# Kernel optimization log

Measured on AMD Instinct MI355X. Metric: run time of the kernel, lower is better.

The kernel has to match this reference:

```python
import jax, jax.numpy as jnp
import numpy as np

DIM = 768
MID = 256
HEADS = 12
P_SCALE = 0.8
SCALE = (DIM // HEADS) ** -0.5


def setup_inputs() -> dict:
    key = jax.random.key(0)
    ks = jax.random.split(key, 9)
    B, N, C = 64, 197, DIM
    s = 0.02
    return {
        "x": jax.random.normal(ks[0], (B, N, C), jnp.float32),
        "qkv_w": jax.random.normal(ks[1], (3 * C, C), jnp.float32) * s,
        "qkv_b": jax.random.normal(ks[2], (3 * C,), jnp.float32) * s,
        "proj_w": jax.random.normal(ks[3], (C, C), jnp.float32) * s,
        "proj_b": jax.random.normal(ks[4], (C,), jnp.float32) * s,
        "down_w": jax.random.normal(ks[5], (MID, C), jnp.float32) * s,
        "down_b": jax.random.normal(ks[6], (MID,), jnp.float32) * s,
        "up_w": jax.random.normal(ks[7], (2 * C, MID), jnp.float32) * s,
        "up_b": jax.random.normal(ks[8], (2 * C,), jnp.float32) * s,
    }


def reference(x, qkv_w, qkv_b, proj_w, proj_b, down_w, down_b, up_w, up_b):
    B, N, C = x.shape
    H, D = HEADS, C // HEADS
    # Adapter: down -> tanh -> up gives kv prefix; q prefix is zeros
    kv_prefix = jnp.tanh(x @ down_w.T + down_b) @ up_w.T + up_b  # [B,N,2C]
    prefix = jnp.concatenate([jnp.zeros((B, N, C), x.dtype), kv_prefix], -1)
    qkv = (x @ qkv_w.T + qkv_b) + P_SCALE * prefix  # [B,N,3C]
    qkv = qkv.reshape(B, N, 3, H, D).transpose(2, 0, 3, 1, 4)  # [3,B,H,N,D]
    q, k, v = qkv[0], qkv[1], qkv[2]
    attn = jax.nn.softmax(jnp.einsum("bhnd,bhmd->bhnm", q, k) * SCALE, axis=-1)
    out = jnp.einsum("bhnm,bhmd->bhnd", attn, v)  # [B,H,N,D]
    out = out.transpose(0, 2, 1, 3).reshape(B, N, C)
    return out @ proj_w.T + proj_b
```

## Files before the change

### kernel.cpp

```cpp
#include <hip/hip_runtime.h>
#include <hip/hip_bf16.h>
#include <stdint.h>

#define DIM   768
#define MID   256
#define HEADS 12
#define NB    64
#define NN    197
#define NT    (NB*NN)
#define QKVC  2304
#define NCOMB 2560

typedef __attribute__((ext_vector_type(4))) float f32x4;
typedef __attribute__((ext_vector_type(8))) short s8v;

__device__ __forceinline__ unsigned short f2b(float f) {
    union { float f; unsigned int u; } x; x.f = f;
    unsigned int u = x.u;
    unsigned int r = (u + 0x7FFFu + ((u >> 16) & 1u)) >> 16;
    return (unsigned short)r;
}
__device__ __forceinline__ float b2f(unsigned short s) {
    union { unsigned int u; float f; } x; x.u = ((unsigned int)s) << 16;
    return x.f;
}

__device__ __forceinline__ void gld_lds16(const void* g, void* l) {
    __builtin_amdgcn_global_load_lds(
        (const __attribute__((address_space(1))) unsigned int*)g,
        (__attribute__((address_space(3))) unsigned int*)l, 16, 0, 0);
}

__global__ void cast_f32_bf16(const float* __restrict__ in,
                              unsigned short* __restrict__ out, int n4) {
    int i = blockIdx.x * blockDim.x + threadIdx.x;
    int stride = gridDim.x * blockDim.x;
    for (; i < n4; i += stride) {
        float4 v = ((const float4*)in)[i];
        ushort4 o;
        o.x = f2b(v.x); o.y = f2b(v.y); o.z = f2b(v.z); o.w = f2b(v.w);
        ((ushort4*)out)[i] = o;
    }
}

__global__ void cast_weights(const float* __restrict__ qkv_w,
                             const float* __restrict__ down_w,
                             const float* __restrict__ up_w,
                             const float* __restrict__ proj_w,
                             unsigned short* __restrict__ o_comb,
                             unsigned short* __restrict__ o_up,
                             unsigned short* __restrict__ o_proj) {
    int blk = blockIdx.x;
    const float* in; unsigned short* out; int base;
    if (blk < 1728)      { in = qkv_w;  out = o_comb;                  base = blk; }
    else if (blk < 1920) { in = down_w; out = o_comb + QKVC * DIM;     base = blk - 1728; }
    else if (blk < 2304) { in = up_w;   out = o_up;                    base = blk - 1920; }
    else                 { in = proj_w; out = o_proj;                  base = blk - 2304; }
    int i = base * 256 + threadIdx.x;
    float4 v = ((const float4*)in)[i];
    ushort4 o;
    o.x = f2b(v.x); o.y = f2b(v.y); o.z = f2b(v.z); o.w = f2b(v.w);
    ((ushort4*)out)[i] = o;
}

__global__ __launch_bounds__(512) void gemm256k64(
    const unsigned short* __restrict__ A,
    const unsigned short* __restrict__ W,
    const float* __restrict__ bias0,
    const float* __restrict__ bias1,
    int M, int K, int GN,
    unsigned short* __restrict__ qkvbuf,
    unsigned short* __restrict__ hbuf)
{
    __shared__ __align__(16) unsigned short As[2][256][64];
    __shared__ __align__(16) unsigned short Bs[2][256][64];
    const int tid = threadIdx.x;
    const int l = tid & 63;
    const int w = tid >> 6;
    const int wr = w >> 2, wc = w & 3;

    const int nwg = gridDim.x;
    const int orig = blockIdx.x;
    const int q8 = nwg >> 3, r8 = nwg & 7;
    const int xcd = orig & 7, slice = orig >> 3;
    const int wgid = (xcd < r8 ? xcd * (q8 + 1)
                               : r8 * (q8 + 1) + (xcd - r8) * q8) + slice;
    const int bm = wgid / GN;
    const int bn = wgid - bm * GN;

    f32x4 acc[8][4];
#pragma unroll
    for (int m = 0; m < 8; ++m)
#pragma unroll
        for (int n = 0; n < 4; ++n)
            acc[m][n] = (f32x4){0.f, 0.f, 0.f, 0.f};

    const int KT = K >> 6;
    const int sc = (((tid & 7) ^ ((tid >> 3) & 7)) << 3);
    const int dc = ((tid & 7) << 3);
    const int rr = tid >> 3;

    auto stage = [&](int buf, int kt) {
        const int k0 = kt << 6;
#pragma unroll
        for (int p = 0; p < 4; ++p) {
            int r = p * 64 + rr;
            int ra = bm * 256 + r; if (ra > M - 1) ra = M - 1;
            gld_lds16(A + (size_t)ra * K + k0 + sc, &As[buf][r][dc]);
            int rb = bn * 256 + r;
            gld_lds16(W + (size_t)rb * K + k0 + sc, &Bs[buf][r][dc]);
        }
    };

    stage(0, 0);

    const int ar  = l & 15;
    const int ch0 = (((l >> 4)    ) ^ (l & 7)) << 3;
    const int ch1 = (((l >> 4) + 4) ^ (l & 7)) << 3;

    for (int t = 0; t < KT; ++t) {
        const int cur = t & 1;
        if (t + 1 < KT) {
            stage(cur ^ 1, t + 1);
            asm volatile("s_waitcnt vmcnt(8)" ::: "memory");
        } else {
            asm volatile("s_waitcnt vmcnt(0)" ::: "memory");
        }
        __builtin_amdgcn_s_barrier();
#pragma unroll
        for (int kk = 0; kk < 2; ++kk) {
            const int ch = kk ? ch1 : ch0;
            s8v a[8], b[4];
#pragma unroll
            for (int m = 0; m < 8; ++m)
                a[m] = *(const s8v*)&As[cur][wr * 128 + m * 16 + ar][ch];
#pragma unroll
            for (int n = 0; n < 4; ++n)
                b[n] = *(const s8v*)&Bs[cur][wc * 64 + n * 16 + ar][ch];
            __builtin_amdgcn_s_setprio(1);
#pragma unroll
            for (int m = 0; m < 8; ++m)
#pragma unroll
                for (int n = 0; n < 4; ++n)
                    acc[m][n] = __builtin_amdgcn_mfma_f32_16x16x32_bf16(a[m], b[n], acc[m][n], 0, 0, 0);
            __builtin_amdgcn_s_setprio(0);
        }
        __builtin_amdgcn_s_barrier();
    }
    asm volatile("s_waitcnt vmcnt(0)" ::: "memory");
    __builtin_amdgcn_s_barrier();

    unsigned short* stg = ((unsigned short*)&As[0][0][0]) + w * (16 * 68);
    const int cbase = bn * 256 + wc * 64;
    const bool ish = (cbase >= QKVC);
#pragma unroll
    for (int mq = 0; mq < 8; ++mq) {
#pragma unroll
        for (int n = 0; n < 4; ++n) {
            int c = cbase + n * 16 + (l & 15);
            float bi = ish ? bias1[c - QKVC] : bias0[c];
            float sc2 = (c < DIM) ? 0.125f : 1.0f;
#pragma unroll
            for (int j = 0; j < 4; ++j) {
                float v = acc[mq][n][j] + bi;
                v = ish ? tanhf(v) : v * sc2;
                stg[((l >> 4) * 4 + j) * 68 + n * 16 + (l & 15)] = f2b(v);
            }
        }
#pragma unroll
        for (int p = 0; p < 2; ++p) {
            int rr2 = p * 8 + (l >> 3);
            int r = bm * 256 + wr * 128 + mq * 16 + rr2;
            s8v v = *(const s8v*)&stg[rr2 * 68 + (l & 7) * 8];
            if (r < M) {
                if (!ish) *(s8v*)&qkvbuf[(size_t)r * QKVC + cbase + (l & 7) * 8] = v;
                else      *(s8v*)&hbuf[(size_t)r * MID + (cbase - QKVC) + (l & 7) * 8] = v;
            }
        }
    }
}

template<int EPI>
__global__ __launch_bounds__(256) void gemm_bt(
    const unsigned short* __restrict__ A,
    const unsigned short* __restrict__ W,
    const float* __restrict__ bias,
    int M, int K, int GN,
    unsigned short* __restrict__ qkvbuf,
    float* __restrict__ outf)
{
    __shared__ __align__(16) unsigned short lds[2][2][128 * 32];
    const int tid = threadIdx.x;
    const int l = tid & 63;
    const int w = tid >> 6;
    const int wr = w >> 1, wc = w & 1;

    const int nwg = gridDim.x;
    const int orig = blockIdx.x;
    const int q8 = nwg >> 3, r8 = nwg & 7;
    const int xcd = orig & 7, slice = orig >> 3;
    const int wgid = (xcd < r8 ? xcd * (q8 + 1)
                               : r8 * (q8 + 1) + (xcd - r8) * q8) + slice;
    const int bm = wgid / GN;
    const int bn = wgid - bm * GN;

    f32x4 acc[4][4];
#pragma unroll
    for (int m = 0; m < 4; ++m)
#pragma unroll
        for (int n = 0; n < 4; ++n)
            acc[m][n] = (f32x4){0.f, 0.f, 0.f, 0.f};

    const int KT = K >> 5;

    auto stage = [&](int buf, int kt) {
        const int k0 = kt * 32;
        const int src = (((tid & 3) ^ ((tid >> 3) & 3)) << 3);
        const int dst = ((tid & 3) << 3);
#pragma unroll
        for (int p = 0; p < 2; ++p) {
            int r = p * 64 + (tid >> 2);
            int ra = bm * 128 + r; if (ra > M - 1) ra = M - 1;
            gld_lds16(A + (size_t)ra * K + k0 + src, &lds[buf][0][r * 32 + dst]);
            int rb = bn * 128 + r;
            gld_lds16(W + (size_t)rb * K + k0 + src, &lds[buf][1][r * 32 + dst]);
        }
    };

    stage(0, 0);
    __syncthreads();
    int buf = 0;
    const int rsl = (((l >> 4) ^ ((l >> 1) & 3)) << 3);
    for (int kt = 0; kt < KT; ++kt) {
        if (kt + 1 < KT) stage(buf ^ 1, kt + 1);
        const unsigned short* la = lds[buf][0];
        const unsigned short* lb = lds[buf][1];
        s8v a[4], b[4];
#pragma unroll
        for (int m = 0; m < 4; ++m)
            a[m] = *(const s8v*)&la[(wr * 64 + m * 16 + (l & 15)) * 32 + rsl];
#pragma unroll
        for (int n = 0; n < 4; ++n)
            b[n] = *(const s8v*)&lb[(wc * 64 + n * 16 + (l & 15)) * 32 + rsl];
#pragma unroll
        for (int m = 0; m < 4; ++m)
#pragma unroll
            for (int n = 0; n < 4; ++n)
                acc[m][n] = __builtin_amdgcn_mfma_f32_16x16x32_bf16(a[m], b[n], acc[m][n], 0, 0, 0);
        __syncthreads();
        buf ^= 1;
    }

    if (EPI == 1) {
        unsigned short* stg = ((unsigned short*)lds) + w * (16 * 68);
        const int C0 = bn * 128 + wc * 64;
#pragma unroll
        for (int mq = 0; mq < 4; ++mq) {
#pragma unroll
            for (int n = 0; n < 4; ++n) {
                int c = C0 + n * 16 + (l & 15);
                float bi = bias[c];
#pragma unroll
                for (int j = 0; j < 4; ++j)
                    stg[((l >> 4) * 4 + j) * 68 + n * 16 + (l & 15)] =
                        f2b(0.8f * (acc[mq][n][j] + bi));
            }
#pragma unroll
            for (int p = 0; p < 2; ++p) {
                int rr2 = p * 8 + (l >> 3);
                int r = bm * 128 + wr * 64 + mq * 16 + rr2;
                if (r < M) {
                    size_t base = (size_t)r * QKVC + DIM + C0 + (l & 7) * 8;
                    s8v add = *(const s8v*)&stg[rr2 * 68 + (l & 7) * 8];
                    s8v old = *(const s8v*)&qkvbuf[base];
                    s8v res;
#pragma unroll
                    for (int i = 0; i < 8; ++i)
                        res[i] = (short)f2b(b2f((unsigned short)old[i]) +
                                            b2f((unsigned short)add[i]));
                    *(s8v*)&qkvbuf[base] = res;
                }
            }
        }
    } else {
#pragma unroll
        for (int n = 0; n < 4; ++n) {
            int c = bn * 128 + wc * 64 + n * 16 + (l & 15);
            float bi = bias[c];
#pragma unroll
            for (int m = 0; m < 4; ++m) {
#pragma unroll
                for (int j = 0; j < 4; ++j) {
                    int r = bm * 128 + wr * 64 + m * 16 + (l >> 4) * 4 + j;
                    if (r >= M) continue;
                    outf[(size_t)r * DIM + c] = acc[m][n][j] + bi;
                }
            }
        }
    }
}

#define NKV  224
#define VPAD 232

__global__ __launch_bounds__(256) void attn_kernel(
    const unsigned short* __restrict__ qkv,
    unsigned short* __restrict__ ob)
{
    __shared__ __align__(16) unsigned short Ks[NKV * 64];
    __shared__ __align__(16) unsigned short Vt[64 * VPAD];
    __shared__ __align__(16) unsigned short Ps[64 * VPAD];

    const int tid = threadIdx.x;
    const int l = tid & 63;
    const int w = tid >> 6;
    const int bh = blockIdx.x;
    const int b = bh / HEADS, h = bh - b * HEADS;
    const unsigned short* qp = qkv + (size_t)(b * NN) * QKVC + h * 64;
    const unsigned short* kp = qp + DIM;
    const unsigned short* vp = qp + 2 * DIM;

    const s8v zer = (s8v){0, 0, 0, 0, 0, 0, 0, 0};

    for (int e = tid; e < NKV * 8; e += 256) {
        int r = e >> 3, ch = e & 7;
        int idx = (r * 64 + ch * 8) ^ ((r & 7) << 3);
        s8v val = (r < NN) ? *(const s8v*)&kp[(size_t)r * QKVC + ch * 8] : zer;
        *(s8v*)&Ks[idx] = val;
    }
    for (int e = tid; e < NKV * 8; e += 256) {
        int r = e >> 3, ch = e & 7;
        s8v val = (r < NN) ? *(const s8v*)&vp[(size_t)r * QKVC + ch * 8] : zer;
#pragma unroll
        for (int i = 0; i < 8; ++i)
            Vt[(ch * 8 + i) * VPAD + r] = (unsigned short)val[i];
    }
    __syncthreads();

    for (int qc = 0; qc < 4; ++qc) {
        const int rbase = qc * 64 + w * 16;
        s8v aq[2];
#pragma unroll
        for (int kc = 0; kc < 2; ++kc) {
            int r = rbase + (l & 15); if (r > NN - 1) r = NN - 1;
            aq[kc] = *(const s8v*)&qp[(size_t)r * QKVC + kc * 32 + (l >> 4) * 8];
        }
        f32x4 sacc[14];
#pragma unroll
        for (int t = 0; t < 14; ++t) sacc[t] = (f32x4){0.f, 0.f, 0.f, 0.f};
#pragma unroll
        for (int t = 0; t < 14; ++t) {
            int col = t * 16 + (l & 15);
#pragma unroll
            for (int kc = 0; kc < 2; ++kc) {
                int idx = (col * 64 + kc * 32 + (l >> 4) * 8) ^ ((col & 7) << 3);
                s8v bk = *(const s8v*)&Ks[idx];
                sacc[t] = __builtin_amdgcn_mfma_f32_16x16x32_bf16(aq[kc], bk, sacc[t], 0, 0, 0);
            }
        }
        float mx[4] = {-1e30f, -1e30f, -1e30f, -1e30f};
#pragma unroll
        for (int t = 0; t < 14; ++t) {
            int col = t * 16 + (l & 15);
            if (col < NN) {
#pragma unroll
                for (int j = 0; j < 4; ++j) mx[j] = fmaxf(mx[j], sacc[t][j]);
            }
        }
#pragma unroll
        for (int j = 0; j < 4; ++j)
#pragma unroll
            for (int off = 1; off < 16; off <<= 1)
                mx[j] = fmaxf(mx[j], __shfl_xor(mx[j], off, 64));

        float sm[4] = {0.f, 0.f, 0.f, 0.f};
#pragma unroll
        for (int t = 0; t < 14; ++t) {
            int col = t * 16 + (l & 15);
#pragma unroll
            for (int j = 0; j < 4; ++j) {
                float p = (col < NN) ? __expf(sacc[t][j] - mx[j]) : 0.f;
                sm[j] += p;
                Ps[(w * 16 + (l >> 4) * 4 + j) * VPAD + col] = f2b(p);
            }
        }
#pragma unroll
        for (int j = 0; j < 4; ++j)
#pragma unroll
            for (int off = 1; off < 16; off <<= 1)
                sm[j] += __shfl_xor(sm[j], off, 64);

        f32x4 oacc[4];
#pragma unroll
        for (int n = 0; n < 4; ++n) oacc[n] = (f32x4){0.f, 0.f, 0.f, 0.f};
#pragma unroll
        for (int kc = 0; kc < 7; ++kc) {
            s8v ap = *(const s8v*)&Ps[(w * 16 + (l & 15)) * VPAD + kc * 32 + (l >> 4) * 8];
#pragma unroll
            for (int n = 0; n < 4; ++n) {
                s8v bv = *(const s8v*)&Vt[(n * 16 + (l & 15)) * VPAD + kc * 32 + (l >> 4) * 8];
                oacc[n] = __builtin_amdgcn_mfma_f32_16x16x32_bf16(ap, bv, oacc[n], 0, 0, 0);
            }
        }
#pragma unroll
        for (int n = 0; n < 4; ++n) {
#pragma unroll
            for (int j = 0; j < 4; ++j) {
                int r = rbase + (l >> 4) * 4 + j;
                if (r < NN) {
                    float val = oacc[n][j] / sm[j];
                    ob[((size_t)(b * NN + r)) * DIM + h * 64 + n * 16 + (l & 15)] = f2b(val);
                }
            }
        }
    }
}

extern "C" void kernel_launch(void* const* d_in, const int* in_sizes, int n_in,
                              void* d_out, int out_size, void* d_ws, size_t ws_size,
                              hipStream_t stream) {
    const float* x      = (const float*)d_in[0];
    const float* qkv_w  = (const float*)d_in[1];
    const float* qkv_b  = (const float*)d_in[2];
    const float* proj_w = (const float*)d_in[3];
    const float* proj_b = (const float*)d_in[4];
    const float* down_w = (const float*)d_in[5];
    const float* down_b = (const float*)d_in[6];
    const float* up_w   = (const float*)d_in[7];
    const float* up_b   = (const float*)d_in[8];
    float* out = (float*)d_out;

    char* ws = (char*)d_ws;
    size_t off = 0;
    unsigned short* xb      = (unsigned short*)(ws + off); off += (size_t)NT * DIM * 2;
    unsigned short* wcomb   = (unsigned short*)(ws + off); off += (size_t)NCOMB * DIM * 2;
    unsigned short* up_wb   = (unsigned short*)(ws + off); off += (size_t)2 * DIM * MID * 2;
    unsigned short* proj_wb = (unsigned short*)(ws + off); off += (size_t)DIM * DIM * 2;
    unsigned short* hbuf    = (unsigned short*)(ws + off); off += (size_t)NT * MID * 2;
    unsigned short* qkvbuf  = (unsigned short*)(ws + off); off += (size_t)NT * QKVC * 2;
    unsigned short* obuf    = xb;

    cast_f32_bf16<<<2048, 256, 0, stream>>>(x, xb, NT * DIM / 4);
    cast_weights<<<2880, 256, 0, stream>>>(qkv_w, down_w, up_w, proj_w,
                                           wcomb, up_wb, proj_wb);

    const int GM1 = (NT + 127) / 128;
    const int GM2 = (NT + 255) / 256;
    gemm256k64<<<GM2 * (NCOMB / 256), 512, 0, stream>>>(xb, wcomb, qkv_b, down_b,
                                                        NT, DIM, NCOMB / 256, qkvbuf, hbuf);
    gemm_bt<1><<<GM1 * (2 * DIM / 128), 256, 0, stream>>>(hbuf, up_wb, up_b, NT, MID, 2 * DIM / 128,
                                                          qkvbuf, nullptr);
    attn_kernel<<<NB * HEADS, 256, 0, stream>>>(qkvbuf, obuf);
    gemm_bt<2><<<GM1 * (DIM / 128), 256, 0, stream>>>(obuf, proj_wb, proj_b, NT, DIM, DIM / 128,
                                                      nullptr, out);
}
```

Baseline: 230.9 us.

## Replace 256x256 QKV/down GEMM with generic 128x128 gemm_bt kernel

Removes the dedicated 512-thread 256x256-tile GEMM for the fused qkv+down projection and instead runs it through the templated 128x128 gemm_bt kernel with a new epilogue (bias, scale, tanh, split outputs). Smaller tiles give about four times as many workgroups, which improves load balance, but reduce operand reuse per byte loaded. The biases are now passed as two pointers throughout.

```diff
diff --git a/kernel.cpp b/kernel.cpp
--- a/kernel.cpp
+++ b/kernel.cpp
@@ -63,130 +63,15 @@
     ((ushort4*)out)[i] = o;
 }
 
-__global__ __launch_bounds__(512) void gemm256k64(
+template<int EPI>
+__global__ __launch_bounds__(256) void gemm_bt(
     const unsigned short* __restrict__ A,
     const unsigned short* __restrict__ W,
     const float* __restrict__ bias0,
     const float* __restrict__ bias1,
     int M, int K, int GN,
-    unsigned short* __restrict__ qkvbuf,
-    unsigned short* __restrict__ hbuf)
-{
-    __shared__ __align__(16) unsigned short As[2][256][64];
-    __shared__ __align__(16) unsigned short Bs[2][256][64];
-    const int tid = threadIdx.x;
-    const int l = tid & 63;
-    const int w = tid >> 6;
-    const int wr = w >> 2, wc = w & 3;
-
-    const int nwg = gridDim.x;
-    const int orig = blockIdx.x;
-    const int q8 = nwg >> 3, r8 = nwg & 7;
-    const int xcd = orig & 7, slice = orig >> 3;
-    const int wgid = (xcd < r8 ? xcd * (q8 + 1)
-                               : r8 * (q8 + 1) + (xcd - r8) * q8) + slice;
-    const int bm = wgid / GN;
-    const int bn = wgid - bm * GN;
-
-    f32x4 acc[8][4];
-#pragma unroll
-    for (int m = 0; m < 8; ++m)
-#pragma unroll
-        for (int n = 0; n < 4; ++n)
-            acc[m][n] = (f32x4){0.f, 0.f, 0.f, 0.f};
-
-    const int KT = K >> 6;
-    const int sc = (((tid & 7) ^ ((tid >> 3) & 7)) << 3);
-    const int dc = ((tid & 7) << 3);
-    const int rr = tid >> 3;
-
-    auto stage = [&](int buf, int kt) {
-        const int k0 = kt << 6;
-#pragma unroll
-        for (int p = 0; p < 4; ++p) {
-            int r = p * 64 + rr;
-            int ra = bm * 256 + r; if (ra > M - 1) ra = M - 1;
-            gld_lds16(A + (size_t)ra * K + k0 + sc, &As[buf][r][dc]);
-            int rb = bn * 256 + r;
-            gld_lds16(W + (size_t)rb * K + k0 + sc, &Bs[buf][r][dc]);
-        }
-    };
-
-    stage(0, 0);
-
-    const int ar  = l & 15;
-    const int ch0 = (((l >> 4)    ) ^ (l & 7)) << 3;
-    const int ch1 = (((l >> 4) + 4) ^ (l & 7)) << 3;
-
-    for (int t = 0; t < KT; ++t) {
-        const int cur = t & 1;
-        if (t + 1 < KT) {
-            stage(cur ^ 1, t + 1);
-            asm volatile("s_waitcnt vmcnt(8)" ::: "memory");
-        } else {
-            asm volatile("s_waitcnt vmcnt(0)" ::: "memory");
-        }
-        __builtin_amdgcn_s_barrier();
-#pragma unroll
-        for (int kk = 0; kk < 2; ++kk) {
-            const int ch = kk ? ch1 : ch0;
-            s8v a[8], b[4];
-#pragma unroll
-            for (int m = 0; m < 8; ++m)
-                a[m] = *(const s8v*)&As[cur][wr * 128 + m * 16 + ar][ch];
-#pragma unroll
-            for (int n = 0; n < 4; ++n)
-                b[n] = *(const s8v*)&Bs[cur][wc * 64 + n * 16 + ar][ch];
-            __builtin_amdgcn_s_setprio(1);
-#pragma unroll
-            for (int m = 0; m < 8; ++m)
-#pragma unroll
-                for (int n = 0; n < 4; ++n)
-                    acc[m][n] = __builtin_amdgcn_mfma_f32_16x16x32_bf16(a[m], b[n], acc[m][n], 0, 0, 0);
-            __builtin_amdgcn_s_setprio(0);
-        }
-        __builtin_amdgcn_s_barrier();
-    }
-    asm volatile("s_waitcnt vmcnt(0)" ::: "memory");
-    __builtin_amdgcn_s_barrier();
-
-    unsigned short* stg = ((unsigned short*)&As[0][0][0]) + w * (16 * 68);
-    const int cbase = bn * 256 + wc * 64;
-    const bool ish = (cbase >= QKVC);
-#pragma unroll
-    for (int mq = 0; mq < 8; ++mq) {
-#pragma unroll
-        for (int n = 0; n < 4; ++n) {
-            int c = cbase + n * 16 + (l & 15);
-            float bi = ish ? bias1[c - QKVC] : bias0[c];
-            float sc2 = (c < DIM) ? 0.125f : 1.0f;
-#pragma unroll
-            for (int j = 0; j < 4; ++j) {
-                float v = acc[mq][n][j] + bi;
-                v = ish ? tanhf(v) : v * sc2;
-                stg[((l >> 4) * 4 + j) * 68 + n * 16 + (l & 15)] = f2b(v);
-            }
-        }
-#pragma unroll
-        for (int p = 0; p < 2; ++p) {
-            int rr2 = p * 8 + (l >> 3);
-            int r = bm * 256 + wr * 128 + mq * 16 + rr2;
-            s8v v = *(const s8v*)&stg[rr2 * 68 + (l & 7) * 8];
-            if (r < M) {
-                if (!ish) *(s8v*)&qkvbuf[(size_t)r * QKVC + cbase + (l & 7) * 8] = v;
-                else      *(s8v*)&hbuf[(size_t)r * MID + (cbase - QKVC) + (l & 7) * 8] = v;
-            }
-        }
-    }
-}
-
-template<int EPI>
-__global__ __launch_bounds__(256) void gemm_bt(
-    const unsigned short* __restrict__ A,
-    const unsigned short* __restrict__ W,
-    const float* __restrict__ bias,
-    int M, int K, int GN,
-    unsigned short* __restrict__ qkvbuf,
+    unsigned short* __restrict__ ob0,
+    unsigned short* __restrict__ ob1,
     float* __restrict__ outf)
 {
     __shared__ __align__(16) unsigned short lds[2][2][128 * 32];
@@ -251,15 +136,44 @@
         buf ^= 1;
     }
 
-    if (EPI == 1) {
+    if (EPI == 0) {
         unsigned short* stg = ((unsigned short*)lds) + w * (16 * 68);
         const int C0 = bn * 128 + wc * 64;
+        const bool ish = (C0 >= QKVC);
 #pragma unroll
         for (int mq = 0; mq < 4; ++mq) {
 #pragma unroll
             for (int n = 0; n < 4; ++n) {
                 int c = C0 + n * 16 + (l & 15);
-                float bi = bias[c];
+                float bi = ish ? bias1[c - QKVC] : bias0[c];
+                float sc2 = (c < DIM) ? 0.125f : 1.0f;
+#pragma unroll
+                for (int j = 0; j < 4; ++j) {
+                    float v = acc[mq][n][j] + bi;
+                    v = ish ? tanhf(v) : v * sc2;
+                    stg[((l >> 4) * 4 + j) * 68 + n * 16 + (l & 15)] = f2b(v);
+                }
+            }
+#pragma unroll
+            for (int p = 0; p < 2; ++p) {
+                int rr2 = p * 8 + (l >> 3);
+                int r = bm * 128 + wr * 64 + mq * 16 + rr2;
+                s8v v = *(const s8v*)&stg[rr2 * 68 + (l & 7) * 8];
+                if (r < M) {
+                    if (!ish) *(s8v*)&ob0[(size_t)r * QKVC + C0 + (l & 7) * 8] = v;
+                    else      *(s8v*)&ob1[(size_t)r * MID + (C0 - QKVC) + (l & 7) * 8] = v;
+                }
+            }
+        }
+    } else if (EPI == 1) {
+        unsigned short* stg = ((unsigned short*)lds) + w * (16 * 68);
+        const int C0 = bn * 128 + wc * 64;
+#pragma unroll
+        for (int mq = 0; mq < 4; ++mq) {
+#pragma unroll
+            for (int n = 0; n < 4; ++n) {
+                int c = C0 + n * 16 + (l & 15);
+                float bi = bias0[c];
 #pragma unroll
                 for (int j = 0; j < 4; ++j)
                     stg[((l >> 4) * 4 + j) * 68 + n * 16 + (l & 15)] =
@@ -272,13 +186,13 @@
                 if (r < M) {
                     size_t base = (size_t)r * QKVC + DIM + C0 + (l & 7) * 8;
                     s8v add = *(const s8v*)&stg[rr2 * 68 + (l & 7) * 8];
-                    s8v old = *(const s8v*)&qkvbuf[base];
+                    s8v old = *(const s8v*)&ob0[base];
                     s8v res;
 #pragma unroll
                     for (int i = 0; i < 8; ++i)
                         res[i] = (short)f2b(b2f((unsigned short)old[i]) +
                                             b2f((unsigned short)add[i]));
-                    *(s8v*)&qkvbuf[base] = res;
+                    *(s8v*)&ob0[base] = res;
                 }
             }
         }
@@ -286,7 +200,7 @@
 #pragma unroll
         for (int n = 0; n < 4; ++n) {
             int c = bn * 128 + wc * 64 + n * 16 + (l & 15);
-            float bi = bias[c];
+            float bi = bias0[c];
 #pragma unroll
             for (int m = 0; m < 4; ++m) {
 #pragma unroll
@@ -445,12 +359,14 @@
                                            wcomb, up_wb, proj_wb);
 
     const int GM1 = (NT + 127) / 128;
-    const int GM2 = (NT + 255) / 256;
-    gemm256k64<<<GM2 * (NCOMB / 256), 512, 0, stream>>>(xb, wcomb, qkv_b, down_b,
-                                                        NT, DIM, NCOMB / 256, qkvbuf, hbuf);
-    gemm_bt<1><<<GM1 * (2 * DIM / 128), 256, 0, stream>>>(hbuf, up_wb, up_b, NT, MID, 2 * DIM / 128,
-                                                          qkvbuf, nullptr);
+    gemm_bt<0><<<GM1 * (NCOMB / 128), 256, 0, stream>>>(xb, wcomb, qkv_b, down_b,
+                                                        NT, DIM, NCOMB / 128,
+                                                        qkvbuf, hbuf, nullptr);
+    gemm_bt<1><<<GM1 * (2 * DIM / 128), 256, 0, stream>>>(hbuf, up_wb, up_b, nullptr,
+                                                          NT, MID, 2 * DIM / 128,
+                                                          qkvbuf, nullptr, nullptr);
     attn_kernel<<<NB * HEADS, 256, 0, stream>>>(qkvbuf, obuf);
-    gemm_bt<2><<<GM1 * (DIM / 128), 256, 0, stream>>>(obuf, proj_wb, proj_b, NT, DIM, DIM / 128,
-                                                      nullptr, out);
-}
+    gemm_bt<2><<<GM1 * (DIM / 128), 256, 0, stream>>>(obuf, proj_wb, proj_b, nullptr,
+                                                      NT, DIM, DIM / 128,
+                                                      nullptr, nullptr, out);
+}
```

After: 217.7 us. -5.7%, faster.

## Restructure GEMM pipelines: ping-pong staged 256-tile loop and triple-buffered gemm_bt

Applied to the files above, without the earlier changes.

The main QKV+down GEMM now splits each K-step into four phases. B-tile halves and the next A tiles are loaded between MFMA bursts, with finer barriers, so global-to-LDS traffic interleaves with compute. gemm_bt moves from double to triple buffering with a prefetch distance of two and one barrier per iteration instead of two syncthreads. The goal is to hide load latency behind compute, at the cost of more barriers, more complex vmcnt accounting and extra LDS in gemm_bt.

```diff
diff --git a/kernel.cpp b/kernel.cpp
--- a/kernel.cpp
+++ b/kernel.cpp
@@ -63,17 +63,16 @@
     ((ushort4*)out)[i] = o;
 }
 
-__global__ __launch_bounds__(512) void gemm256k64(
+__global__ __launch_bounds__(512) void gemm256p8(
     const unsigned short* __restrict__ A,
     const unsigned short* __restrict__ W,
     const float* __restrict__ bias0,
     const float* __restrict__ bias1,
     int M, int K, int GN,
-    unsigned short* __restrict__ qkvbuf,
-    unsigned short* __restrict__ hbuf)
+    unsigned short* __restrict__ ob0,
+    unsigned short* __restrict__ ob1)
 {
-    __shared__ __align__(16) unsigned short As[2][256][64];
-    __shared__ __align__(16) unsigned short Bs[2][256][64];
+    __shared__ __align__(16) unsigned short lds[2][4][128 * 64];
     const int tid = threadIdx.x;
     const int l = tid & 63;
     const int w = tid >> 6;
@@ -96,61 +95,117 @@
             acc[m][n] = (f32x4){0.f, 0.f, 0.f, 0.f};
 
     const int KT = K >> 6;
-    const int sc = (((tid & 7) ^ ((tid >> 3) & 7)) << 3);
-    const int dc = ((tid & 7) << 3);
-    const int rr = tid >> 3;
-
-    auto stage = [&](int buf, int kt) {
-        const int k0 = kt << 6;
-#pragma unroll
-        for (int p = 0; p < 4; ++p) {
-            int r = p * 64 + rr;
-            int ra = bm * 256 + r; if (ra > M - 1) ra = M - 1;
-            gld_lds16(A + (size_t)ra * K + k0 + sc, &As[buf][r][dc]);
-            int rb = bn * 256 + r;
-            gld_lds16(W + (size_t)rb * K + k0 + sc, &Bs[buf][r][dc]);
+
+    const int srr = tid >> 3;
+    const int scd = tid & 7;
+    const int scs = (scd ^ (srr & 7)) * 8;
+    const int sld = scd * 8;
+
+    auto stageA = [&](int par, int half, int kt2) {
+        const int k0 = kt2 << 6;
+#pragma unroll
+        for (int i = 0; i < 2; ++i) {
+            int r = srr + i * 64;
+            int ra = bm * 256 + half * 128 + r; if (ra > M - 1) ra = M - 1;
+            gld_lds16(A + (size_t)ra * K + k0 + scs, &lds[par][half][r * 64 + sld]);
         }
     };
-
-    stage(0, 0);
-
-    const int ar  = l & 15;
-    const int ch0 = (((l >> 4)    ) ^ (l & 7)) << 3;
-    const int ch1 = (((l >> 4) + 4) ^ (l & 7)) << 3;
-
-    for (int t = 0; t < KT; ++t) {
-        const int cur = t & 1;
-        if (t + 1 < KT) {
-            stage(cur ^ 1, t + 1);
-            asm volatile("s_waitcnt vmcnt(8)" ::: "memory");
+    auto stageB = [&](int par, int half, int kt2) {
+        const int k0 = kt2 << 6;
+#pragma unroll
+        for (int i = 0; i < 2; ++i) {
+            int r = srr + i * 64;
+            int rb = bn * 256 + half * 128 + r;
+            gld_lds16(W + (size_t)rb * K + k0 + scs, &lds[par][2 + half][r * 64 + sld]);
+        }
+    };
+
+    stageA(0, 0, 0); stageA(0, 1, 0); stageB(0, 0, 0); stageB(0, 1, 0);
+    if (KT > 1) { stageA(1, 0, 1); stageA(1, 1, 1);
+                  asm volatile("s_waitcnt vmcnt(4)" ::: "memory"); }
+    else        { asm volatile("s_waitcnt vmcnt(0)" ::: "memory"); }
+    __builtin_amdgcn_s_barrier();
+    asm volatile("" ::: "memory");
+
+    const int r15 = l & 15;
+    const int cA0 = ((l >> 4) ^ (l & 7)) * 8;
+    const int cA1 = (((l >> 4) + 4) ^ (l & 7)) * 8;
+    const int aro = r15 * 64;
+    const int bro = ((wc & 1) * 64 + r15) * 64;
+
+    for (int kt = 0; kt < KT; ++kt) {
+        const int p = kt & 1;
+        const unsigned short* Ah = &lds[p][wr][0];
+        const unsigned short* Bh = &lds[p][2 + (wc >> 1)][0];
+        s8v a[8], b0, b1;
+
+#pragma unroll
+        for (int m = 0; m < 8; ++m)
+            a[m] = *(const s8v*)&Ah[aro + m * 1024 + cA0];
+        b0 = *(const s8v*)&Bh[bro + 0 * 1024 + cA0];
+        b1 = *(const s8v*)&Bh[bro + 1 * 1024 + cA0];
+        if (kt + 1 < KT) stageB(p ^ 1, 0, kt + 1);
+        __builtin_amdgcn_s_barrier();
+        __builtin_amdgcn_s_setprio(1);
+#pragma unroll
+        for (int m = 0; m < 8; ++m) {
+            acc[m][0] = __builtin_amdgcn_mfma_f32_16x16x32_bf16(a[m], b0, acc[m][0], 0, 0, 0);
+            acc[m][1] = __builtin_amdgcn_mfma_f32_16x16x32_bf16(a[m], b1, acc[m][1], 0, 0, 0);
+        }
+        __builtin_amdgcn_s_setprio(0);
+        __builtin_amdgcn_s_barrier();
+
+        b0 = *(const s8v*)&Bh[bro + 2 * 1024 + cA0];
+        b1 = *(const s8v*)&Bh[bro + 3 * 1024 + cA0];
+        if (kt + 1 < KT) stageB(p ^ 1, 1, kt + 1);
+        __builtin_amdgcn_s_barrier();
+        __builtin_amdgcn_s_setprio(1);
+#pragma unroll
+        for (int m = 0; m < 8; ++m) {
+            acc[m][2] = __builtin_amdgcn_mfma_f32_16x16x32_bf16(a[m], b0, acc[m][2], 0, 0, 0);
+            acc[m][3] = __builtin_amdgcn_mfma_f32_16x16x32_bf16(a[m], b1, acc[m][3], 0, 0, 0);
+        }
+        __builtin_amdgcn_s_setprio(0);
+        __builtin_amdgcn_s_barrier();
+
+#pragma unroll
+        for (int m = 0; m < 8; ++m)
+            a[m] = *(const s8v*)&Ah[aro + m * 1024 + cA1];
+        b0 = *(const s8v*)&Bh[bro + 0 * 1024 + cA1];
+        b1 = *(const s8v*)&Bh[bro + 1 * 1024 + cA1];
+        __builtin_amdgcn_s_barrier();
+        __builtin_amdgcn_s_setprio(1);
+#pragma unroll
+        for (int m = 0; m < 8; ++m) {
+            acc[m][0] = __builtin_amdgcn_mfma_f32_16x16x32_bf16(a[m], b0, acc[m][0], 0, 0, 0);
+            acc[m][1] = __builtin_amdgcn_mfma_f32_16x16x32_bf16(a[m], b1, acc[m][1], 0, 0, 0);
+        }
+        __builtin_amdgcn_s_setprio(0);
+        __builtin_amdgcn_s_barrier();
+
+        b0 = *(const s8v*)&Bh[bro + 2 * 1024 + cA1];
+        b1 = *(const s8v*)&Bh[bro + 3 * 1024 + cA1];
+        if (kt + 2 < KT) {
+            stageA(p, 0, kt + 2); stageA(p, 1, kt + 2);
+            asm volatile("s_waitcnt vmcnt(4)" ::: "memory");
         } else {
             asm volatile("s_waitcnt vmcnt(0)" ::: "memory");
         }
         __builtin_amdgcn_s_barrier();
-#pragma unroll
-        for (int kk = 0; kk < 2; ++kk) {
-            const int ch = kk ? ch1 : ch0;
-            s8v a[8], b[4];
-#pragma unroll
-            for (int m = 0; m < 8; ++m)
-                a[m] = *(const s8v*)&As[cur][wr * 128 + m * 16 + ar][ch];
-#pragma unroll
-            for (int n = 0; n < 4; ++n)
-                b[n] = *(const s8v*)&Bs[cur][wc * 64 + n * 16 + ar][ch];
-            __builtin_amdgcn_s_setprio(1);
-#pragma unroll
-            for (int m = 0; m < 8; ++m)
-#pragma unroll
-                for (int n = 0; n < 4; ++n)
-                    acc[m][n] = __builtin_amdgcn_mfma_f32_16x16x32_bf16(a[m], b[n], acc[m][n], 0, 0, 0);
-            __builtin_amdgcn_s_setprio(0);
-        }
-        __builtin_amdgcn_s_barrier();
-    }
+        __builtin_amdgcn_s_setprio(1);
+#pragma unroll
+        for (int m = 0; m < 8; ++m) {
+            acc[m][2] = __builtin_amdgcn_mfma_f32_16x16x32_bf16(a[m], b0, acc[m][2], 0, 0, 0);
+            acc[m][3] = __builtin_amdgcn_mfma_f32_16x16x32_bf16(a[m], b1, acc[m][3], 0, 0, 0);
+        }
+        __builtin_amdgcn_s_setprio(0);
+        __builtin_amdgcn_s_barrier();
+        asm volatile("" ::: "memory");
+    }
+
     asm volatile("s_waitcnt vmcnt(0)" ::: "memory");
-    __builtin_amdgcn_s_barrier();
-
-    unsigned short* stg = ((unsigned short*)&As[0][0][0]) + w * (16 * 68);
+    __syncthreads();
+    unsigned short* stg = ((unsigned short*)lds) + w * (16 * 68);
     const int cbase = bn * 256 + wc * 64;
     const bool ish = (cbase >= QKVC);
 #pragma unroll
@@ -168,13 +223,13 @@
             }
         }
 #pragma unroll
-        for (int p = 0; p < 2; ++p) {
-            int rr2 = p * 8 + (l >> 3);
+        for (int p2 = 0; p2 < 2; ++p2) {
+            int rr2 = p2 * 8 + (l >> 3);
             int r = bm * 256 + wr * 128 + mq * 16 + rr2;
             s8v v = *(const s8v*)&stg[rr2 * 68 + (l & 7) * 8];
             if (r < M) {
-                if (!ish) *(s8v*)&qkvbuf[(size_t)r * QKVC + cbase + (l & 7) * 8] = v;
-                else      *(s8v*)&hbuf[(size_t)r * MID + (cbase - QKVC) + (l & 7) * 8] = v;
+                if (!ish) *(s8v*)&ob0[(size_t)r * QKVC + cbase + (l & 7) * 8] = v;
+                else      *(s8v*)&ob1[(size_t)r * MID + (cbase - QKVC) + (l & 7) * 8] = v;
             }
         }
     }
@@ -184,12 +239,12 @@
 __global__ __launch_bounds__(256) void gemm_bt(
     const unsigned short* __restrict__ A,
     const unsigned short* __restrict__ W,
-    const float* __restrict__ bias,
+    const float* __restrict__ bias0,
     int M, int K, int GN,
-    unsigned short* __restrict__ qkvbuf,
+    unsigned short* __restrict__ ob0,
     float* __restrict__ outf)
 {
-    __shared__ __align__(16) unsigned short lds[2][2][128 * 32];
+    __shared__ __align__(16) unsigned short lds[3][2][128 * 32];
     const int tid = threadIdx.x;
     const int l = tid & 63;
     const int w = tid >> 6;
@@ -228,13 +283,19 @@
     };
 
     stage(0, 0);
-    __syncthreads();
-    int buf = 0;
+    stage(1, 1);
+
     const int rsl = (((l >> 4) ^ ((l >> 1) & 3)) << 3);
+    int cb = 0;
+    int sb = 2;
     for (int kt = 0; kt < KT; ++kt) {
-        if (kt + 1 < KT) stage(buf ^ 1, kt + 1);
-        const unsigned short* la = lds[buf][0];
-        const unsigned short* lb = lds[buf][1];
+        if (kt + 1 < KT) asm volatile("s_waitcnt vmcnt(4)" ::: "memory");
+        else             asm volatile("s_waitcnt vmcnt(0)" ::: "memory");
+        __builtin_amdgcn_s_barrier();
+        asm volatile("" ::: "memory");
+        if (kt + 2 < KT) stage(sb, kt + 2);
+        const unsigned short* la = lds[cb][0];
+        const unsigned short* lb = lds[cb][1];
         s8v a[4], b[4];
 #pragma unroll
         for (int m = 0; m < 4; ++m)
@@ -247,9 +308,10 @@
 #pragma unroll
             for (int n = 0; n < 4; ++n)
                 acc[m][n] = __builtin_amdgcn_mfma_f32_16x16x32_bf16(a[m], b[n], acc[m][n], 0, 0, 0);
-        __syncthreads();
-        buf ^= 1;
-    }
+        cb = (cb == 2) ? 0 : cb + 1;
+        sb = (sb == 2) ? 0 : sb + 1;
+    }
+    __syncthreads();
 
     if (EPI == 1) {
         unsigned short* stg = ((unsigned short*)lds) + w * (16 * 68);
@@ -259,7 +321,7 @@
 #pragma unroll
             for (int n = 0; n < 4; ++n) {
                 int c = C0 + n * 16 + (l & 15);
-                float bi = bias[c];
+                float bi = bias0[c];
 #pragma unroll
                 for (int j = 0; j < 4; ++j)
                     stg[((l >> 4) * 4 + j) * 68 + n * 16 + (l & 15)] =
@@ -272,13 +334,13 @@
                 if (r < M) {
                     size_t base = (size_t)r * QKVC + DIM + C0 + (l & 7) * 8;
                     s8v add = *(const s8v*)&stg[rr2 * 68 + (l & 7) * 8];
-                    s8v old = *(const s8v*)&qkvbuf[base];
+                    s8v old = *(const s8v*)&ob0[base];
                     s8v res;
 #pragma unroll
                     for (int i = 0; i < 8; ++i)
                         res[i] = (short)f2b(b2f((unsigned short)old[i]) +
                                             b2f((unsigned short)add[i]));
-                    *(s8v*)&qkvbuf[base] = res;
+                    *(s8v*)&ob0[base] = res;
                 }
             }
         }
@@ -286,7 +348,7 @@
 #pragma unroll
         for (int n = 0; n < 4; ++n) {
             int c = bn * 128 + wc * 64 + n * 16 + (l & 15);
-            float bi = bias[c];
+            float bi = bias0[c];
 #pragma unroll
             for (int m = 0; m < 4; ++m) {
 #pragma unroll
@@ -446,8 +508,8 @@
 
     const int GM1 = (NT + 127) / 128;
     const int GM2 = (NT + 255) / 256;
-    gemm256k64<<<GM2 * (NCOMB / 256), 512, 0, stream>>>(xb, wcomb, qkv_b, down_b,
-                                                        NT, DIM, NCOMB / 256, qkvbuf, hbuf);
+    gemm256p8<<<GM2 * (NCOMB / 256), 512, 0, stream>>>(xb, wcomb, qkv_b, down_b,
+                                                       NT, DIM, NCOMB / 256, qkvbuf, hbuf);
     gemm_bt<1><<<GM1 * (2 * DIM / 128), 256, 0, stream>>>(hbuf, up_wb, up_b, NT, MID, 2 * DIM / 128,
                                                           qkvbuf, nullptr);
     attn_kernel<<<NB * HEADS, 256, 0, stream>>>(qkvbuf, obuf);
```

Measured after the change: 230.4 us. No clear change (-0.2%).

## Retile combined GEMM to 256x128 and triple-buffer LDS pipelines

Applied to the files above, without the earlier changes.

The combined QKV+down GEMM drops its 256x256, K=64, 512-thread tile for a 256x128, K=32 tile with 256 threads and two blocks per CU. Both it and gemm_bt now use a three-stage LDS ring with prefetch distance two and a single barrier per k-step. The goal is to hide global-to-LDS latency and raise occupancy, removing the second per-iteration barrier. In exchange there are more k-iterations and more A-tile reloads, since each A tile is now read by twice as many column blocks.

```diff
diff --git a/kernel.cpp b/kernel.cpp
--- a/kernel.cpp
+++ b/kernel.cpp
@@ -63,21 +63,20 @@
     ((ushort4*)out)[i] = o;
 }
 
-__global__ __launch_bounds__(512) void gemm256k64(
+__global__ __launch_bounds__(256, 2) void gemm_comb(
     const unsigned short* __restrict__ A,
     const unsigned short* __restrict__ W,
     const float* __restrict__ bias0,
     const float* __restrict__ bias1,
     int M, int K, int GN,
-    unsigned short* __restrict__ qkvbuf,
-    unsigned short* __restrict__ hbuf)
+    unsigned short* __restrict__ ob0,
+    unsigned short* __restrict__ ob1)
 {
-    __shared__ __align__(16) unsigned short As[2][256][64];
-    __shared__ __align__(16) unsigned short Bs[2][256][64];
+    __shared__ __align__(16) unsigned short lds[3][384 * 32];
     const int tid = threadIdx.x;
     const int l = tid & 63;
     const int w = tid >> 6;
-    const int wr = w >> 2, wc = w & 3;
+    const int wr = w >> 1, wc = w & 1;
 
     const int nwg = gridDim.x;
     const int orig = blockIdx.x;
@@ -95,63 +94,61 @@
         for (int n = 0; n < 4; ++n)
             acc[m][n] = (f32x4){0.f, 0.f, 0.f, 0.f};
 
-    const int KT = K >> 6;
-    const int sc = (((tid & 7) ^ ((tid >> 3) & 7)) << 3);
-    const int dc = ((tid & 7) << 3);
-    const int rr = tid >> 3;
+    const int KT = K >> 5;
 
     auto stage = [&](int buf, int kt) {
-        const int k0 = kt << 6;
+        const int k0 = kt * 32;
+        const int src = (((tid & 3) ^ ((tid >> 3) & 3)) << 3);
+        const int dst = ((tid & 3) << 3);
 #pragma unroll
         for (int p = 0; p < 4; ++p) {
-            int r = p * 64 + rr;
+            int r = p * 64 + (tid >> 2);
             int ra = bm * 256 + r; if (ra > M - 1) ra = M - 1;
-            gld_lds16(A + (size_t)ra * K + k0 + sc, &As[buf][r][dc]);
-            int rb = bn * 256 + r;
-            gld_lds16(W + (size_t)rb * K + k0 + sc, &Bs[buf][r][dc]);
+            gld_lds16(A + (size_t)ra * K + k0 + src, &lds[buf][r * 32 + dst]);
+        }
+#pragma unroll
+        for (int p = 0; p < 2; ++p) {
+            int r = p * 64 + (tid >> 2);
+            int rb = bn * 128 + r;
+            gld_lds16(W + (size_t)rb * K + k0 + src, &lds[buf][8192 + r * 32 + dst]);
         }
     };
 
     stage(0, 0);
-
-    const int ar  = l & 15;
-    const int ch0 = (((l >> 4)    ) ^ (l & 7)) << 3;
-    const int ch1 = (((l >> 4) + 4) ^ (l & 7)) << 3;
-
-    for (int t = 0; t < KT; ++t) {
-        const int cur = t & 1;
-        if (t + 1 < KT) {
-            stage(cur ^ 1, t + 1);
-            asm volatile("s_waitcnt vmcnt(8)" ::: "memory");
-        } else {
-            asm volatile("s_waitcnt vmcnt(0)" ::: "memory");
-        }
+    stage(1, 1);
+
+    const int rsl = (((l >> 4) ^ ((l >> 1) & 3)) << 3);
+    int cb = 0;
+    int sb = 2;
+    for (int kt = 0; kt < KT; ++kt) {
+        if (kt + 1 < KT) asm volatile("s_waitcnt vmcnt(6)" ::: "memory");
+        else             asm volatile("s_waitcnt vmcnt(0)" ::: "memory");
         __builtin_amdgcn_s_barrier();
-#pragma unroll
-        for (int kk = 0; kk < 2; ++kk) {
-            const int ch = kk ? ch1 : ch0;
-            s8v a[8], b[4];
-#pragma unroll
-            for (int m = 0; m < 8; ++m)
-                a[m] = *(const s8v*)&As[cur][wr * 128 + m * 16 + ar][ch];
+        asm volatile("" ::: "memory");
+        if (kt + 2 < KT) stage(sb, kt + 2);
+        const unsigned short* la = &lds[cb][0];
+        const unsigned short* lb = &lds[cb][8192];
+        s8v a[8], b[4];
+#pragma unroll
+        for (int m = 0; m < 8; ++m)
+            a[m] = *(const s8v*)&la[(wr * 128 + m * 16 + (l & 15)) * 32 + rsl];
+#pragma unroll
+        for (int n = 0; n < 4; ++n)
+            b[n] = *(const s8v*)&lb[(wc * 64 + n * 16 + (l & 15)) * 32 + rsl];
+        __builtin_amdgcn_s_setprio(1);
+#pragma unroll
+        for (int m = 0; m < 8; ++m)
 #pragma unroll
             for (int n = 0; n < 4; ++n)
-                b[n] = *(const s8v*)&Bs[cur][wc * 64 + n * 16 + ar][ch];
-            __builtin_amdgcn_s_setprio(1);
-#pragma unroll
-            for (int m = 0; m < 8; ++m)
-#pragma unroll
-                for (int n = 0; n < 4; ++n)
-                    acc[m][n] = __builtin_amdgcn_mfma_f32_16x16x32_bf16(a[m], b[n], acc[m][n], 0, 0, 0);
-            __builtin_amdgcn_s_setprio(0);
-        }
-        __builtin_amdgcn_s_barrier();
-    }
-    asm volatile("s_waitcnt vmcnt(0)" ::: "memory");
-    __builtin_amdgcn_s_barrier();
-
-    unsigned short* stg = ((unsigned short*)&As[0][0][0]) + w * (16 * 68);
-    const int cbase = bn * 256 + wc * 64;
+                acc[m][n] = __builtin_amdgcn_mfma_f32_16x16x32_bf16(a[m], b[n], acc[m][n], 0, 0, 0);
+        __builtin_amdgcn_s_setprio(0);
+        cb = (cb == 2) ? 0 : cb + 1;
+        sb = (sb == 2) ? 0 : sb + 1;
+    }
+    __syncthreads();
+
+    unsigned short* stg = ((unsigned short*)lds) + w * (16 * 68);
+    const int cbase = bn * 128 + wc * 64;
     const bool ish = (cbase >= QKVC);
 #pragma unroll
     for (int mq = 0; mq < 8; ++mq) {
@@ -168,13 +165,13 @@
             }
         }
 #pragma unroll
-        for (int p = 0; p < 2; ++p) {
-            int rr2 = p * 8 + (l >> 3);
+        for (int p2 = 0; p2 < 2; ++p2) {
+            int rr2 = p2 * 8 + (l >> 3);
             int r = bm * 256 + wr * 128 + mq * 16 + rr2;
             s8v v = *(const s8v*)&stg[rr2 * 68 + (l & 7) * 8];
             if (r < M) {
-                if (!ish) *(s8v*)&qkvbuf[(size_t)r * QKVC + cbase + (l & 7) * 8] = v;
-                else      *(s8v*)&hbuf[(size_t)r * MID + (cbase - QKVC) + (l & 7) * 8] = v;
+                if (!ish) *(s8v*)&ob0[(size_t)r * QKVC + cbase + (l & 7) * 8] = v;
+                else      *(s8v*)&ob1[(size_t)r * MID + (cbase - QKVC) + (l & 7) * 8] = v;
             }
         }
     }
@@ -184,12 +181,12 @@
 __global__ __launch_bounds__(256) void gemm_bt(
     const unsigned short* __restrict__ A,
     const unsigned short* __restrict__ W,
-    const float* __restrict__ bias,
+    const float* __restrict__ bias0,
     int M, int K, int GN,
-    unsigned short* __restrict__ qkvbuf,
+    unsigned short* __restrict__ ob0,
     float* __restrict__ outf)
 {
-    __shared__ __align__(16) unsigned short lds[2][2][128 * 32];
+    __shared__ __align__(16) unsigned short lds[3][2][128 * 32];
     const int tid = threadIdx.x;
     const int l = tid & 63;
     const int w = tid >> 6;
@@ -228,13 +225,19 @@
     };
 
     stage(0, 0);
-    __syncthreads();
-    int buf = 0;
+    stage(1, 1);
+
     const int rsl = (((l >> 4) ^ ((l >> 1) & 3)) << 3);
+    int cb = 0;
+    int sb = 2;
     for (int kt = 0; kt < KT; ++kt) {
-        if (kt + 1 < KT) stage(buf ^ 1, kt + 1);
-        const unsigned short* la = lds[buf][0];
-        const unsigned short* lb = lds[buf][1];
+        if (kt + 1 < KT) asm volatile("s_waitcnt vmcnt(4)" ::: "memory");
+        else             asm volatile("s_waitcnt vmcnt(0)" ::: "memory");
+        __builtin_amdgcn_s_barrier();
+        asm volatile("" ::: "memory");
+        if (kt + 2 < KT) stage(sb, kt + 2);
+        const unsigned short* la = lds[cb][0];
+        const unsigned short* lb = lds[cb][1];
         s8v a[4], b[4];
 #pragma unroll
         for (int m = 0; m < 4; ++m)
@@ -247,9 +250,10 @@
 #pragma unroll
             for (int n = 0; n < 4; ++n)
                 acc[m][n] = __builtin_amdgcn_mfma_f32_16x16x32_bf16(a[m], b[n], acc[m][n], 0, 0, 0);
-        __syncthreads();
-        buf ^= 1;
-    }
+        cb = (cb == 2) ? 0 : cb + 1;
+        sb = (sb == 2) ? 0 : sb + 1;
+    }
+    __syncthreads();
 
     if (EPI == 1) {
         unsigned short* stg = ((unsigned short*)lds) + w * (16 * 68);
@@ -259,7 +263,7 @@
 #pragma unroll
             for (int n = 0; n < 4; ++n) {
                 int c = C0 + n * 16 + (l & 15);
-                float bi = bias[c];
+                float bi = bias0[c];
 #pragma unroll
                 for (int j = 0; j < 4; ++j)
                     stg[((l >> 4) * 4 + j) * 68 + n * 16 + (l & 15)] =
@@ -272,13 +276,13 @@
                 if (r < M) {
                     size_t base = (size_t)r * QKVC + DIM + C0 + (l & 7) * 8;
                     s8v add = *(const s8v*)&stg[rr2 * 68 + (l & 7) * 8];
-                    s8v old = *(const s8v*)&qkvbuf[base];
+                    s8v old = *(const s8v*)&ob0[base];
                     s8v res;
 #pragma unroll
                     for (int i = 0; i < 8; ++i)
                         res[i] = (short)f2b(b2f((unsigned short)old[i]) +
                                             b2f((unsigned short)add[i]));
-                    *(s8v*)&qkvbuf[base] = res;
+                    *(s8v*)&ob0[base] = res;
                 }
             }
         }
@@ -286,7 +290,7 @@
 #pragma unroll
         for (int n = 0; n < 4; ++n) {
             int c = bn * 128 + wc * 64 + n * 16 + (l & 15);
-            float bi = bias[c];
+            float bi = bias0[c];
 #pragma unroll
             for (int m = 0; m < 4; ++m) {
 #pragma unroll
@@ -446,8 +450,9 @@
 
     const int GM1 = (NT + 127) / 128;
     const int GM2 = (NT + 255) / 256;
-    gemm256k64<<<GM2 * (NCOMB / 256), 512, 0, stream>>>(xb, wcomb, qkv_b, down_b,
-                                                        NT, DIM, NCOMB / 256, qkvbuf, hbuf);
+    gemm_comb<<<GM2 * (NCOMB / 128), 256, 0, stream>>>(xb, wcomb, qkv_b, down_b,
+                                                       NT, DIM, NCOMB / 128,
+                                                       qkvbuf, hbuf);
     gemm_bt<1><<<GM1 * (2 * DIM / 128), 256, 0, stream>>>(hbuf, up_wb, up_b, NT, MID, 2 * DIM / 128,
                                                           qkvbuf, nullptr);
     attn_kernel<<<NB * HEADS, 256, 0, stream>>>(qkvbuf, obuf);
```

After: 230.0 us. About the same (-0.4%).
